# Performance work log

Hardware: AMD Instinct MI355X
Metric: run time of the kernel (lower is better)

## Reference

```python
import jax, jax.numpy as jnp
import numpy as np

B, S, HID = 2, 2048, 1024
NH, NKV, HD = 16, 8, 128
EPS = 1e-6
THETA = 1.0e6
NEG = -1e9

def _rope_tables():
    inv_freq = 1.0 / (THETA ** (np.arange(0, HD, 2, dtype=np.float32) / HD))  # [HD/2]
    pos = np.arange(S, dtype=np.float32)
    freqs = np.outer(pos, inv_freq)                      # [S, HD/2]
    emb = np.concatenate([freqs, freqs], axis=-1)        # [S, HD]
    cos = np.broadcast_to(np.cos(emb), (B, S, HD)).copy()
    sin = np.broadcast_to(np.sin(emb), (B, S, HD)).copy()
    return jnp.asarray(cos), jnp.asarray(sin)

def setup_inputs() -> dict:
    key = jax.random.key(0)
    ks = jax.random.split(key, 8)
    hidden_states = jax.random.normal(ks[0], (B, S, HID), jnp.float32)
    cos, sin = _rope_tables()
    # additive causal mask [B,1,S,S]
    causal = jnp.triu(jnp.full((S, S), NEG, jnp.float32), k=1)
    attention_mask = jnp.broadcast_to(causal[None, None], (B, 1, S, S))
    std = 0.02
    Wq = jax.random.normal(ks[1], (NH * HD, HID), jnp.float32) * std
    Wk = jax.random.normal(ks[2], (NKV * HD, HID), jnp.float32) * std
    Wv = jax.random.normal(ks[3], (NKV * HD, HID), jnp.float32) * std
    Wo = jax.random.normal(ks[4], (HID, NH * HD), jnp.float32) * std
    q_norm_w = jnp.ones((HD,), jnp.float32)
    k_norm_w = jnp.ones((HD,), jnp.float32)
    return {"hidden_states": hidden_states, "cos": cos, "sin": sin,
            "attention_mask": attention_mask, "Wq": Wq, "Wk": Wk, "Wv": Wv,
            "Wo": Wo, "q_norm_w": q_norm_w, "k_norm_w": k_norm_w}

def _rms_norm(x, w):
    var = jnp.mean(jnp.square(x), axis=-1, keepdims=True)
    return x * jax.lax.rsqrt(var + EPS) * w

def _rotate_half(x):
    x1, x2 = jnp.split(x, 2, axis=-1)
    return jnp.concatenate([-x2, x1], axis=-1)

def reference(hidden_states, cos, sin, attention_mask, Wq, Wk, Wv, Wo, q_norm_w, k_norm_w):
    # projections: [B,S,heads,HD] -> [B,heads,S,HD]
    q = jnp.einsum('bsh,dh->bsd', hidden_states, Wq).reshape(B, S, NH, HD)
    k = jnp.einsum('bsh,dh->bsd', hidden_states, Wk).reshape(B, S, NKV, HD)
    v = jnp.einsum('bsh,dh->bsd', hidden_states, Wv).reshape(B, S, NKV, HD)
    q = jnp.transpose(_rms_norm(q, q_norm_w), (0, 2, 1, 3))
    k = jnp.transpose(_rms_norm(k, k_norm_w), (0, 2, 1, 3))
    v = jnp.transpose(v, (0, 2, 1, 3))
    c = cos[:, None]  # [B,1,S,HD]
    s = sin[:, None]
    q = q * c + _rotate_half(q) * s
    k = k * c + _rotate_half(k) * s
    # repeat kv heads: NKV -> NH
    n_rep = NH // NKV
    k = jnp.repeat(k, n_rep, axis=1)
    v = jnp.repeat(v, n_rep, axis=1)
    scaling = HD ** -0.5
    scores = jnp.einsum('bhqd,bhkd->bhqk', q, k) * scaling
    scores = scores + attention_mask
    probs = jax.nn.softmax(scores.astype(jnp.float32), axis=-1).astype(q.dtype)
    out = jnp.einsum('bhqk,bhkd->bhqd', probs, v)
    out = jnp.transpose(out, (0, 2, 1, 3)).reshape(B, S, NH * HD)
    return jnp.einsum('bsd,hd->bsh', out, Wo)
```

## Files before the change

kernel.cpp:

```cpp
#include <hip/hip_runtime.h>
#include <hip/hip_fp16.h>


typedef _Float16 f16;
typedef __attribute__((ext_vector_type(8))) _Float16 f16x8;
typedef __attribute__((ext_vector_type(4))) _Float16 f16x4;
typedef __attribute__((ext_vector_type(4))) float f32x4;

__constant__ const float kEps = 1e-6f;
__constant__ const float kScaleL2 = 0.1275179120685481f;

#define ASYNC_LD16(gp, lp)                                              \
  __builtin_amdgcn_global_load_lds(                                     \
      (const __attribute__((address_space(1))) void*)(gp),              \
      (__attribute__((address_space(3))) void*)(uint32_t)(uintptr_t)(lp), 16, 0, 0)

__global__ __launch_bounds__(256) void cast_all(
    const float* __restrict__ h, const float* __restrict__ wq,
    const float* __restrict__ wk, const float* __restrict__ wv,
    const float* __restrict__ wo, f16* __restrict__ hb,
    f16* __restrict__ wqkv, f16* __restrict__ wob) {
  const int idx = blockIdx.x * 256 + threadIdx.x;
  const float* src;
  f16* dst;
  int base;
  if (idx < 1048576) { src = h;  dst = hb;                  base = 0; }
  else if (idx < 1572864) { src = wq; dst = wqkv;               base = 1048576; }
  else if (idx < 1835008) { src = wk; dst = wqkv + 2048 * 1024; base = 1572864; }
  else if (idx < 2097152) { src = wv; dst = wqkv + 3072 * 1024; base = 1835008; }
  else { src = wo; dst = wob; base = 2097152; }
  const int i = (idx - base) * 4;
  f32x4 v = *reinterpret_cast<const f32x4*>(src + i);
  f16x4 o;
  o.x = (f16)v.x; o.y = (f16)v.y; o.z = (f16)v.z; o.w = (f16)v.w;
  *reinterpret_cast<f16x4*>(dst + i) = o;
}

__global__ __launch_bounds__(256) void gemm_bt_h(const f16* __restrict__ A,
                                                 const f16* __restrict__ Bm,
                                                 f16* __restrict__ C,
                                                 int M, int N, int K) {
  __shared__ __align__(16) f16 As[128][64];
  __shared__ __align__(16) f16 Bs[128][64];
  const int tid = threadIdx.x;
  const int lane = tid & 63;
  const int wave = tid >> 6;
  const int cl = lane & 15;
  const int quad = lane >> 4;
  const int wm = (wave >> 1) * 64;
  const int wn = (wave & 1) * 64;
  const int tm = blockIdx.y * 128;
  const int tn = blockIdx.x * 128;
  const int r0 = tid >> 3;
  const int csw = ((tid & 7) ^ (r0 & 7)) * 8;

  const f16* Ab = A + (size_t)(tm + r0) * K + csw;
  const f16* Bb = Bm + (size_t)(tn + r0) * K + csw;
  char* Al = (char*)As + wave * 1024;
  char* Bl = (char*)Bs + wave * 1024;

  f32x4 acc[4][4] = {};

  for (int k0 = 0; k0 < K; k0 += 64) {
#pragma unroll
    for (int c = 0; c < 4; ++c) {
      ASYNC_LD16(Ab + (size_t)(c * 32) * K + k0, Al + c * 4096);
      ASYNC_LD16(Bb + (size_t)(c * 32) * K + k0, Bl + c * 4096);
    }
    __syncthreads();
#pragma unroll
    for (int kk = 0; kk < 2; ++kk) {
      f16x8 af[4], bf[4];
#pragma unroll
      for (int mi = 0; mi < 4; ++mi)
        af[mi] = *reinterpret_cast<const f16x8*>(
            &As[wm + mi * 16 + cl][((kk * 4 + quad) ^ (cl & 7)) * 8]);
#pragma unroll
      for (int ni = 0; ni < 4; ++ni)
        bf[ni] = *reinterpret_cast<const f16x8*>(
            &Bs[wn + ni * 16 + cl][((kk * 4 + quad) ^ (cl & 7)) * 8]);
#pragma unroll
      for (int mi = 0; mi < 4; ++mi)
#pragma unroll
        for (int ni = 0; ni < 4; ++ni)
          acc[mi][ni] =
              __builtin_amdgcn_mfma_f32_16x16x32_f16(af[mi], bf[ni], acc[mi][ni], 0, 0, 0);
    }
    __syncthreads();
  }
#pragma unroll
  for (int mi = 0; mi < 4; ++mi)
#pragma unroll
    for (int ni = 0; ni < 4; ++ni)
#pragma unroll
      for (int r = 0; r < 4; ++r)
        C[(size_t)(tm + wm + mi * 16 + quad * 4 + r) * N + tn + wn + ni * 16 + cl] =
            (f16)acc[mi][ni][r];
}

__global__ __launch_bounds__(256) void gemm_bt64(const f16* __restrict__ A,
                                                 const f16* __restrict__ Bm,
                                                 float* __restrict__ C,
                                                 int M, int N, int K) {
  __shared__ __align__(16) f16 As[64][64];
  __shared__ __align__(16) f16 Bs[128][64];
  const int tid = threadIdx.x;
  const int lane = tid & 63;
  const int wave = tid >> 6;
  const int cl = lane & 15;
  const int quad = lane >> 4;
  const int wm = (wave >> 1) * 32;
  const int wn = (wave & 1) * 64;
  const int tm = blockIdx.y * 64;
  const int tn = blockIdx.x * 128;
  const int r0 = tid >> 3;
  const int csw = ((tid & 7) ^ (r0 & 7)) * 8;

  const f16* Ab = A + (size_t)(tm + r0) * K + csw;
  const f16* Bb = Bm + (size_t)(tn + r0) * K + csw;
  char* Al = (char*)As + wave * 1024;
  char* Bl = (char*)Bs + wave * 1024;

  f32x4 acc[2][4] = {};

  for (int k0 = 0; k0 < K; k0 += 64) {
#pragma unroll
    for (int c = 0; c < 2; ++c)
      ASYNC_LD16(Ab + (size_t)(c * 32) * K + k0, Al + c * 4096);
#pragma unroll
    for (int c = 0; c < 4; ++c)
      ASYNC_LD16(Bb + (size_t)(c * 32) * K + k0, Bl + c * 4096);
    __syncthreads();
#pragma unroll
    for (int kk = 0; kk < 2; ++kk) {
      f16x8 af[2], bf[4];
#pragma unroll
      for (int mi = 0; mi < 2; ++mi)
        af[mi] = *reinterpret_cast<const f16x8*>(
            &As[wm + mi * 16 + cl][((kk * 4 + quad) ^ (cl & 7)) * 8]);
#pragma unroll
      for (int ni = 0; ni < 4; ++ni)
        bf[ni] = *reinterpret_cast<const f16x8*>(
            &Bs[wn + ni * 16 + cl][((kk * 4 + quad) ^ (cl & 7)) * 8]);
#pragma unroll
      for (int mi = 0; mi < 2; ++mi)
#pragma unroll
        for (int ni = 0; ni < 4; ++ni)
          acc[mi][ni] =
              __builtin_amdgcn_mfma_f32_16x16x32_f16(af[mi], bf[ni], acc[mi][ni], 0, 0, 0);
    }
    __syncthreads();
  }
#pragma unroll
  for (int mi = 0; mi < 2; ++mi)
#pragma unroll
    for (int ni = 0; ni < 4; ++ni)
#pragma unroll
      for (int r = 0; r < 4; ++r)
        C[(size_t)(tm + wm + mi * 16 + quad * 4 + r) * N + tn + wn + ni * 16 + cl] =
            acc[mi][ni][r];
}

__global__ __launch_bounds__(256) void rope_norm(
    const f16* __restrict__ qkvh,
    const float* __restrict__ cosT, const float* __restrict__ sinT,
    const float* __restrict__ qw, const float* __restrict__ kw,
    f16* __restrict__ qt, f16* __restrict__ kt) {
  const int gw = blockIdx.x * 4 + (threadIdx.x >> 6);
  const int lane = threadIdx.x & 63;
  const int head = gw % 24;
  const int bs = gw / 24;
  const bool isq = head < 16;
  const f16* src = qkvh + (size_t)bs * 4096 +
                   (isq ? head * 128 : 2048 + (head - 16) * 128);
  const float x1 = (float)src[lane];
  const float x2 = (float)src[lane + 64];
  float ss = x1 * x1 + x2 * x2;
#pragma unroll
  for (int off = 32; off >= 1; off >>= 1) ss += __shfl_xor(ss, off);
  const float rms = rsqrtf(ss * (1.0f / 128.0f) + kEps);
  const float* w = isq ? qw : kw;
  const float n1 = x1 * rms * w[lane];
  const float n2 = x2 * rms * w[lane + 64];
  const float* cb = cosT + (size_t)bs * 128;
  const float* sb = sinT + (size_t)bs * 128;
  const float o1 = n1 * cb[lane] - n2 * sb[lane];
  const float o2 = n2 * cb[lane + 64] + n1 * sb[lane + 64];
  const int b = bs >> 11;
  const int s = bs & 2047;
  f16* dst;
  float sc;
  if (isq) {
    dst = qt + ((size_t)(b * 16 + head) * 2048 + s) * 128;
    sc = kScaleL2;
  } else {
    dst = kt + ((size_t)(b * 8 + (head - 16)) * 2048 + s) * 128;
    sc = 1.0f;
  }
  dst[lane] = (f16)(o1 * sc);
  dst[lane + 64] = (f16)(o2 * sc);
}

__global__ __launch_bounds__(256) void v_transpose(const f16* __restrict__ qkvh,
                                                   f16* __restrict__ vt) {
  __shared__ __align__(16) f16 tile[64][136];
  const int bh = blockIdx.y;
  const int b = bh >> 3, h = bh & 7;
  const int s0 = blockIdx.x * 64;
  const int tid = threadIdx.x;
#pragma unroll
  for (int i = 0; i < 4; ++i) {
    int c = tid + i * 256;
    int s = c >> 4;
    int cg = c & 15;
    f16x8 v = *reinterpret_cast<const f16x8*>(
        qkvh + (size_t)(b * 2048 + s0 + s) * 4096 + 3072 + h * 128 + cg * 8);
    *reinterpret_cast<f16x8*>(&tile[s][cg * 8]) = v;
  }
  __syncthreads();
#pragma unroll
  for (int i = 0; i < 4; ++i) {
    int c = tid + i * 256;
    int d = c >> 3;
    int sB = (c & 7) * 8;
    f16x8 o;
#pragma unroll
    for (int j = 0; j < 8; ++j) o[j] = tile[sB + j][d];
    *reinterpret_cast<f16x8*>(vt + ((size_t)(b * 8 + h) * 128 + d) * 2048 + s0 + sB) = o;
  }
}

__global__ __launch_bounds__(128) void attn(const f16* __restrict__ Qt,
                                            const f16* __restrict__ Kt,
                                            const f16* __restrict__ Vt,
                                            f16* __restrict__ Ot) {
  __shared__ __align__(16) f16 Ks[64 * 128];
  __shared__ __align__(16) f16 Vs[128 * 64];
  __shared__ __align__(16) f16 Ps[2][32][72];

  const int bid = blockIdx.x;
  const int bh = bid & 31;
  const int t = 31 - (bid >> 5);
  const int q0 = t * 64;
  const int b = bh >> 4, h = bh & 15;
  const int kv = h >> 1;

  const int tid = threadIdx.x;
  const int lane = tid & 63, wv = tid >> 6;
  const int cl = lane & 15, quad = lane >> 4;
  const int qw0 = q0 + wv * 32;

  const f16* qbase = Qt + ((size_t)(b * 16 + h) * 2048 + qw0 + cl) * 128;
  f16x8 aq[2][4];
#pragma unroll
  for (int mi = 0; mi < 2; ++mi)
#pragma unroll
    for (int kk = 0; kk < 4; ++kk)
      aq[mi][kk] =
          *reinterpret_cast<const f16x8*>(qbase + mi * 16 * 128 + kk * 32 + quad * 8);

  const f16* kbase = Kt + (size_t)(b * 8 + kv) * 2048 * 128;
  const f16* vbase = Vt + (size_t)(b * 8 + kv) * 128 * 2048;

  float m_[2] = {-1e30f, -1e30f}, l_[2] = {0.f, 0.f};
  f32x4 oacc[2][8] = {};

  for (int kt0 = 0; kt0 <= q0; kt0 += 64) {
#pragma unroll
    for (int i = 0; i < 8; ++i) {
      const int c = (wv * 8 + i) * 64 + lane;
      const int kr = c >> 4, kg = c & 15;
      const int kgs = (kg & 8) | ((kg & 7) ^ (kr & 7));
      ASYNC_LD16(kbase + (size_t)(kt0 + kr) * 128 + kgs * 8,
                 (char*)Ks + (wv * 8 + i) * 1024);
      const int vr = c >> 3, vg = c & 7;
      const int vgs = vg ^ (vr & 7);
      ASYNC_LD16(vbase + (size_t)vr * 2048 + kt0 + vgs * 8,
                 (char*)Vs + (wv * 8 + i) * 1024);
    }
    __syncthreads();
    f32x4 sacc[2][4] = {};
#pragma unroll
    for (int kk = 0; kk < 4; ++kk)
#pragma unroll
      for (int ni = 0; ni < 4; ++ni) {
        const int gk = kk * 4 + quad;
        const int gks = (gk & 8) | ((gk & 7) ^ (cl & 7));
        f16x8 ak =
            *reinterpret_cast<const f16x8*>(Ks + (ni * 16 + cl) * 128 + gks * 8);
#pragma unroll
        for (int mi = 0; mi < 2; ++mi)
          sacc[mi][ni] =
              __builtin_amdgcn_mfma_f32_16x16x32_f16(ak, aq[mi][kk], sacc[mi][ni], 0, 0, 0);
      }
    if (kt0 == q0) {
#pragma unroll
      for (int mi = 0; mi < 2; ++mi) {
        const int qg = qw0 + mi * 16 + cl;
#pragma unroll
        for (int ni = 0; ni < 4; ++ni) {
          const int sg = kt0 + ni * 16 + quad * 4;
#pragma unroll
          for (int r = 0; r < 4; ++r)
            if (sg + r > qg) sacc[mi][ni][r] = -1e30f;
        }
      }
    }
    float al[2];
#pragma unroll
    for (int mi = 0; mi < 2; ++mi) {
      float m0 = sacc[mi][0][0];
#pragma unroll
      for (int ni = 0; ni < 4; ++ni)
#pragma unroll
        for (int r = 0; r < 4; ++r) m0 = fmaxf(m0, sacc[mi][ni][r]);
      m0 = fmaxf(m0, __shfl_xor(m0, 16));
      m0 = fmaxf(m0, __shfl_xor(m0, 32));
      const float nm = fmaxf(m_[mi], m0);
      al[mi] = __builtin_amdgcn_exp2f(m_[mi] - nm);
      m_[mi] = nm;
      float ps = 0.f;
#pragma unroll
      for (int ni = 0; ni < 4; ++ni)
#pragma unroll
        for (int r = 0; r < 4; ++r) {
          const float p = __builtin_amdgcn_exp2f(sacc[mi][ni][r] - nm);
          sacc[mi][ni][r] = p;
          ps += p;
        }
      l_[mi] = l_[mi] * al[mi] + ps;
    }
#pragma unroll
    for (int mi = 0; mi < 2; ++mi)
#pragma unroll
      for (int ni = 0; ni < 4; ++ni) {
        f16x4 pk;
#pragma unroll
        for (int r = 0; r < 4; ++r) pk[r] = (f16)sacc[mi][ni][r];
        *reinterpret_cast<f16x4*>(&Ps[wv][mi * 16 + cl][ni * 16 + quad * 4]) = pk;
      }
#pragma unroll
    for (int mi = 0; mi < 2; ++mi)
#pragma unroll
      for (int dg = 0; dg < 8; ++dg) oacc[mi][dg] *= al[mi];
    asm volatile("s_waitcnt lgkmcnt(0)" ::: "memory");
    f16x8 bp[2][2];
#pragma unroll
    for (int mi = 0; mi < 2; ++mi)
#pragma unroll
      for (int kh = 0; kh < 2; ++kh)
        bp[mi][kh] =
            *reinterpret_cast<const f16x8*>(&Ps[wv][mi * 16 + cl][kh * 32 + quad * 8]);
#pragma unroll
    for (int kh = 0; kh < 2; ++kh)
#pragma unroll
      for (int dg = 0; dg < 8; ++dg) {
        const int gv = kh * 4 + quad;
        const int gvs = gv ^ (cl & 7);
        f16x8 av =
            *reinterpret_cast<const f16x8*>(Vs + (dg * 16 + cl) * 64 + gvs * 8);
#pragma unroll
        for (int mi = 0; mi < 2; ++mi)
          oacc[mi][dg] =
              __builtin_amdgcn_mfma_f32_16x16x32_f16(av, bp[mi][kh], oacc[mi][dg], 0, 0, 0);
      }
    __syncthreads();
  }
#pragma unroll
  for (int mi = 0; mi < 2; ++mi) {
    float l = l_[mi];
    l += __shfl_xor(l, 16);
    l += __shfl_xor(l, 32);
    const float inv = 1.0f / l;
    const size_t qg = qw0 + mi * 16 + cl;
#pragma unroll
    for (int dg = 0; dg < 8; ++dg) {
      f16x4 o;
#pragma unroll
      for (int r = 0; r < 4; ++r) o[r] = (f16)(oacc[mi][dg][r] * inv);
      *reinterpret_cast<f16x4*>(Ot + ((size_t)b * 2048 + qg) * 2048 + h * 128 +
                                dg * 16 + quad * 4) = o;
    }
  }
}

extern "C" void kernel_launch(void* const* d_in, const int* in_sizes, int n_in,
                              void* d_out, int out_size, void* d_ws, size_t ws_size,
                              hipStream_t stream) {
  (void)in_sizes; (void)n_in; (void)out_size; (void)ws_size;
  const float* hidden = (const float*)d_in[0];
  const float* cosT = (const float*)d_in[1];
  const float* sinT = (const float*)d_in[2];
  const float* Wq = (const float*)d_in[4];
  const float* Wk = (const float*)d_in[5];
  const float* Wv = (const float*)d_in[6];
  const float* Wo = (const float*)d_in[7];
  const float* qnw = (const float*)d_in[8];
  const float* knw = (const float*)d_in[9];
  float* out = (float*)d_out;

  char* ws = (char*)d_ws;
  size_t off = 0;
  auto alloc = [&](size_t bytes) {
    char* p = ws + off;
    off += (bytes + 255) & ~(size_t)255;
    return p;
  };
  f16* hb = (f16*)alloc(4096ull * 1024 * 2);
  f16* wqkv = (f16*)alloc(4096ull * 1024 * 2);
  f16* wob = (f16*)alloc(1024ull * 2048 * 2);
  f16* qkvh = (f16*)alloc(4096ull * 4096 * 2);
  f16* qt = (f16*)alloc(32ull * 2048 * 128 * 2);
  f16* kt = (f16*)alloc(16ull * 2048 * 128 * 2);
  f16* vt = (f16*)alloc(16ull * 2048 * 128 * 2);
  f16* ot = (f16*)alloc(4096ull * 2048 * 2);

  cast_all<<<10240, 256, 0, stream>>>(hidden, Wq, Wk, Wv, Wo, hb, wqkv, wob);

  gemm_bt_h<<<dim3(32, 32), 256, 0, stream>>>(hb, wqkv, qkvh, 4096, 4096, 1024);

  rope_norm<<<24576, 256, 0, stream>>>(qkvh, cosT, sinT, qnw, knw, qt, kt);
  v_transpose<<<dim3(32, 16), 256, 0, stream>>>(qkvh, vt);

  attn<<<1024, 128, 0, stream>>>(qt, kt, vt, ot);

  gemm_bt64<<<dim3(8, 64), 256, 0, stream>>>(ot, wob, out, 4096, 1024, 2048);
}
```

Baseline: 302.6 us.

## Double-buffer K/V tiles in attention with async prefetch and MFMA priority

The attention kernel now keeps two LDS buffers for K and V and issues the async global-to-LDS loads for the next key tile before computing on the current one. Waits use explicit vmcnt counts so only the older loads are drained, and raw s_barrier replaces __syncthreads. s_setprio is raised around the MFMA blocks, and the causal-mask condition is tightened to apply per wave. LDS use doubles, from 32KB to 64KB for K/V, which may lower occupancy.

After: 313.9 us. 1.04x slower.

```diff
diff --git a/kernel.cpp b/kernel.cpp
--- a/kernel.cpp
+++ b/kernel.cpp
@@ -234,8 +234,8 @@
                                             const f16* __restrict__ Kt,
                                             const f16* __restrict__ Vt,
                                             f16* __restrict__ Ot) {
-  __shared__ __align__(16) f16 Ks[64 * 128];
-  __shared__ __align__(16) f16 Vs[128 * 64];
+  __shared__ __align__(16) f16 Ks[2][64 * 128];
+  __shared__ __align__(16) f16 Vs[2][128 * 64];
   __shared__ __align__(16) f16 Ps[2][32][72];
 
   const int bid = blockIdx.x;
@@ -262,24 +262,40 @@
   const f16* kbase = Kt + (size_t)(b * 8 + kv) * 2048 * 128;
   const f16* vbase = Vt + (size_t)(b * 8 + kv) * 128 * 2048;
 
-  float m_[2] = {-1e30f, -1e30f}, l_[2] = {0.f, 0.f};
-  f32x4 oacc[2][8] = {};
-
-  for (int kt0 = 0; kt0 <= q0; kt0 += 64) {
+  auto stage = [&](int buf, int kt0) {
 #pragma unroll
     for (int i = 0; i < 8; ++i) {
-      const int c = (wv * 8 + i) * 64 + lane;
+      const int cc = wv * 8 + i;
+      const int c = cc * 64 + lane;
       const int kr = c >> 4, kg = c & 15;
       const int kgs = (kg & 8) | ((kg & 7) ^ (kr & 7));
       ASYNC_LD16(kbase + (size_t)(kt0 + kr) * 128 + kgs * 8,
-                 (char*)Ks + (wv * 8 + i) * 1024);
+                 (char*)Ks + buf * 16384 + cc * 1024);
       const int vr = c >> 3, vg = c & 7;
       const int vgs = vg ^ (vr & 7);
       ASYNC_LD16(vbase + (size_t)vr * 2048 + kt0 + vgs * 8,
-                 (char*)Vs + (wv * 8 + i) * 1024);
-    }
-    __syncthreads();
+                 (char*)Vs + buf * 16384 + cc * 1024);
+    }
+  };
+
+  float m_[2] = {-1e30f, -1e30f}, l_[2] = {0.f, 0.f};
+  f32x4 oacc[2][8] = {};
+
+  stage(0, 0);
+  int cur = 0;
+  for (int kt0 = 0; kt0 <= q0; kt0 += 64) {
+    const bool hasNext = (kt0 + 64 <= q0);
+    if (hasNext) {
+      stage(cur ^ 1, kt0 + 64);
+      asm volatile("s_waitcnt vmcnt(16)" ::: "memory");
+    } else {
+      asm volatile("s_waitcnt vmcnt(0)" ::: "memory");
+    }
+    __builtin_amdgcn_s_barrier();
+    const f16* Kc = &Ks[cur][0];
+    const f16* Vc = &Vs[cur][0];
     f32x4 sacc[2][4] = {};
+    __builtin_amdgcn_s_setprio(1);
 #pragma unroll
     for (int kk = 0; kk < 4; ++kk)
 #pragma unroll
@@ -287,13 +303,14 @@
         const int gk = kk * 4 + quad;
         const int gks = (gk & 8) | ((gk & 7) ^ (cl & 7));
         f16x8 ak =
-            *reinterpret_cast<const f16x8*>(Ks + (ni * 16 + cl) * 128 + gks * 8);
+            *reinterpret_cast<const f16x8*>(Kc + (ni * 16 + cl) * 128 + gks * 8);
 #pragma unroll
         for (int mi = 0; mi < 2; ++mi)
           sacc[mi][ni] =
               __builtin_amdgcn_mfma_f32_16x16x32_f16(ak, aq[mi][kk], sacc[mi][ni], 0, 0, 0);
       }
-    if (kt0 == q0) {
+    __builtin_amdgcn_s_setprio(0);
+    if (kt0 + 63 > qw0) {
 #pragma unroll
       for (int mi = 0; mi < 2; ++mi) {
         const int qg = qw0 + mi * 16 + cl;
@@ -351,6 +368,7 @@
       for (int kh = 0; kh < 2; ++kh)
         bp[mi][kh] =
             *reinterpret_cast<const f16x8*>(&Ps[wv][mi * 16 + cl][kh * 32 + quad * 8]);
+    __builtin_amdgcn_s_setprio(1);
 #pragma unroll
     for (int kh = 0; kh < 2; ++kh)
 #pragma unroll
@@ -358,13 +376,15 @@
         const int gv = kh * 4 + quad;
         const int gvs = gv ^ (cl & 7);
         f16x8 av =
-            *reinterpret_cast<const f16x8*>(Vs + (dg * 16 + cl) * 64 + gvs * 8);
+            *reinterpret_cast<const f16x8*>(Vc + (dg * 16 + cl) * 64 + gvs * 8);
 #pragma unroll
         for (int mi = 0; mi < 2; ++mi)
           oacc[mi][dg] =
               __builtin_amdgcn_mfma_f32_16x16x32_f16(av, bp[mi][kh], oacc[mi][dg], 0, 0, 0);
       }
-    __syncthreads();
+    __builtin_amdgcn_s_setprio(0);
+    __builtin_amdgcn_s_barrier();
+    cur ^= 1;
   }
 #pragma unroll
   for (int mi = 0; mi < 2; ++mi) {
```

## Load V fragments directly into registers instead of staging through LDS

Applied to the files above, without the earlier changes.

The attention kernel no longer copies the V tile into shared memory. Each lane now reads its own V MFMA operands straight from global memory into registers, issuing the two halves at different points so the loads can overlap the QK^T MFMAs. s_setprio is raised around the MFMA sections, and the causal mask is now applied per wave whenever the tile crosses that wave's diagonal. This cuts LDS traffic and frees shared memory for occupancy, at the cost of more VGPRs and uncoalesced, duplicated global reads of V (both waves fetch the same data).

Result: slower. 319.4 us (+5.6%).

```diff
diff --git a/kernel.cpp b/kernel.cpp
--- a/kernel.cpp
+++ b/kernel.cpp
@@ -235,7 +235,6 @@
                                             const f16* __restrict__ Vt,
                                             f16* __restrict__ Ot) {
   __shared__ __align__(16) f16 Ks[64 * 128];
-  __shared__ __align__(16) f16 Vs[128 * 64];
   __shared__ __align__(16) f16 Ps[2][32][72];
 
   const int bid = blockIdx.x;
@@ -260,26 +259,29 @@
           *reinterpret_cast<const f16x8*>(qbase + mi * 16 * 128 + kk * 32 + quad * 8);
 
   const f16* kbase = Kt + (size_t)(b * 8 + kv) * 2048 * 128;
-  const f16* vbase = Vt + (size_t)(b * 8 + kv) * 128 * 2048;
+  const f16* vlane = Vt + (size_t)(b * 8 + kv) * 128 * 2048 + (size_t)cl * 2048 +
+                     quad * 8;
 
   float m_[2] = {-1e30f, -1e30f}, l_[2] = {0.f, 0.f};
   f32x4 oacc[2][8] = {};
 
   for (int kt0 = 0; kt0 <= q0; kt0 += 64) {
+    f16x8 av0[8];
+#pragma unroll
+    for (int dg = 0; dg < 8; ++dg)
+      av0[dg] = *reinterpret_cast<const f16x8*>(vlane + (size_t)(dg * 16) * 2048 + kt0);
 #pragma unroll
     for (int i = 0; i < 8; ++i) {
-      const int c = (wv * 8 + i) * 64 + lane;
+      const int cc = wv * 8 + i;
+      const int c = cc * 64 + lane;
       const int kr = c >> 4, kg = c & 15;
       const int kgs = (kg & 8) | ((kg & 7) ^ (kr & 7));
       ASYNC_LD16(kbase + (size_t)(kt0 + kr) * 128 + kgs * 8,
-                 (char*)Ks + (wv * 8 + i) * 1024);
-      const int vr = c >> 3, vg = c & 7;
-      const int vgs = vg ^ (vr & 7);
-      ASYNC_LD16(vbase + (size_t)vr * 2048 + kt0 + vgs * 8,
-                 (char*)Vs + (wv * 8 + i) * 1024);
+                 (char*)Ks + cc * 1024);
     }
     __syncthreads();
     f32x4 sacc[2][4] = {};
+    __builtin_amdgcn_s_setprio(1);
 #pragma unroll
     for (int kk = 0; kk < 4; ++kk)
 #pragma unroll
@@ -293,7 +295,13 @@
           sacc[mi][ni] =
               __builtin_amdgcn_mfma_f32_16x16x32_f16(ak, aq[mi][kk], sacc[mi][ni], 0, 0, 0);
       }
-    if (kt0 == q0) {
+    __builtin_amdgcn_s_setprio(0);
+    f16x8 av1[8];
+#pragma unroll
+    for (int dg = 0; dg < 8; ++dg)
+      av1[dg] =
+          *reinterpret_cast<const f16x8*>(vlane + (size_t)(dg * 16) * 2048 + kt0 + 32);
+    if (kt0 + 63 > qw0) {
 #pragma unroll
       for (int mi = 0; mi < 2; ++mi) {
         const int qg = qw0 + mi * 16 + cl;
@@ -351,19 +359,20 @@
       for (int kh = 0; kh < 2; ++kh)
         bp[mi][kh] =
             *reinterpret_cast<const f16x8*>(&Ps[wv][mi * 16 + cl][kh * 32 + quad * 8]);
-#pragma unroll
-    for (int kh = 0; kh < 2; ++kh)
-#pragma unroll
-      for (int dg = 0; dg < 8; ++dg) {
-        const int gv = kh * 4 + quad;
-        const int gvs = gv ^ (cl & 7);
-        f16x8 av =
-            *reinterpret_cast<const f16x8*>(Vs + (dg * 16 + cl) * 64 + gvs * 8);
-#pragma unroll
-        for (int mi = 0; mi < 2; ++mi)
-          oacc[mi][dg] =
-              __builtin_amdgcn_mfma_f32_16x16x32_f16(av, bp[mi][kh], oacc[mi][dg], 0, 0, 0);
-      }
+    __builtin_amdgcn_s_setprio(1);
+#pragma unroll
+    for (int dg = 0; dg < 8; ++dg)
+#pragma unroll
+      for (int mi = 0; mi < 2; ++mi)
+        oacc[mi][dg] =
+            __builtin_amdgcn_mfma_f32_16x16x32_f16(av0[dg], bp[mi][0], oacc[mi][dg], 0, 0, 0);
+#pragma unroll
+    for (int dg = 0; dg < 8; ++dg)
+#pragma unroll
+      for (int mi = 0; mi < 2; ++mi)
+        oacc[mi][dg] =
+            __builtin_amdgcn_mfma_f32_16x16x32_f16(av1[dg], bp[mi][1], oacc[mi][dg], 0, 0, 0);
+    __builtin_amdgcn_s_setprio(0);
     __syncthreads();
   }
 #pragma unroll
```

## Split attention query tile across four waves and raise MFMA priority

Applied to the files above, without the earlier changes.

The attention kernel now runs 256 threads per block, so each of four waves owns 16 query rows instead of two waves owning 32 each. Per-wave accumulators, softmax state and the P scratch tile are halved, and the K/V tile loads are spread over more threads. The causal-mask test moves to per-wave granularity, and s_setprio is raised around the MFMA loops. More waves per block means more latency hiding and lower register pressure, but each K/V tile loaded into LDS is reused by fewer MFMAs per wave.

Measured after the change: 294.0 us. 1.03x faster.

```diff
diff --git a/kernel.cpp b/kernel.cpp
--- a/kernel.cpp
+++ b/kernel.cpp
@@ -230,13 +230,13 @@
   }
 }
 
-__global__ __launch_bounds__(128) void attn(const f16* __restrict__ Qt,
-                                            const f16* __restrict__ Kt,
-                                            const f16* __restrict__ Vt,
-                                            f16* __restrict__ Ot) {
+__global__ __launch_bounds__(256, 3) void attn(const f16* __restrict__ Qt,
+                                               const f16* __restrict__ Kt,
+                                               const f16* __restrict__ Vt,
+                                               f16* __restrict__ Ot) {
   __shared__ __align__(16) f16 Ks[64 * 128];
   __shared__ __align__(16) f16 Vs[128 * 64];
-  __shared__ __align__(16) f16 Ps[2][32][72];
+  __shared__ __align__(16) f16 Ps[4][16][72];
 
   const int bid = blockIdx.x;
   const int bh = bid & 31;
@@ -248,109 +248,94 @@
   const int tid = threadIdx.x;
   const int lane = tid & 63, wv = tid >> 6;
   const int cl = lane & 15, quad = lane >> 4;
-  const int qw0 = q0 + wv * 32;
+  const int qw0 = q0 + wv * 16;
 
   const f16* qbase = Qt + ((size_t)(b * 16 + h) * 2048 + qw0 + cl) * 128;
-  f16x8 aq[2][4];
-#pragma unroll
-  for (int mi = 0; mi < 2; ++mi)
-#pragma unroll
-    for (int kk = 0; kk < 4; ++kk)
-      aq[mi][kk] =
-          *reinterpret_cast<const f16x8*>(qbase + mi * 16 * 128 + kk * 32 + quad * 8);
+  f16x8 aq[4];
+#pragma unroll
+  for (int kk = 0; kk < 4; ++kk)
+    aq[kk] = *reinterpret_cast<const f16x8*>(qbase + kk * 32 + quad * 8);
 
   const f16* kbase = Kt + (size_t)(b * 8 + kv) * 2048 * 128;
   const f16* vbase = Vt + (size_t)(b * 8 + kv) * 128 * 2048;
 
-  float m_[2] = {-1e30f, -1e30f}, l_[2] = {0.f, 0.f};
-  f32x4 oacc[2][8] = {};
+  float m_ = -1e30f, l_ = 0.f;
+  f32x4 oacc[8] = {};
 
   for (int kt0 = 0; kt0 <= q0; kt0 += 64) {
 #pragma unroll
-    for (int i = 0; i < 8; ++i) {
-      const int c = (wv * 8 + i) * 64 + lane;
+    for (int i = 0; i < 4; ++i) {
+      const int c = i * 256 + tid;
       const int kr = c >> 4, kg = c & 15;
       const int kgs = (kg & 8) | ((kg & 7) ^ (kr & 7));
       ASYNC_LD16(kbase + (size_t)(kt0 + kr) * 128 + kgs * 8,
-                 (char*)Ks + (wv * 8 + i) * 1024);
+                 (char*)Ks + i * 4096 + wv * 1024);
       const int vr = c >> 3, vg = c & 7;
       const int vgs = vg ^ (vr & 7);
       ASYNC_LD16(vbase + (size_t)vr * 2048 + kt0 + vgs * 8,
-                 (char*)Vs + (wv * 8 + i) * 1024);
-    }
-    __syncthreads();
-    f32x4 sacc[2][4] = {};
-#pragma unroll
-    for (int kk = 0; kk < 4; ++kk)
+                 (char*)Vs + i * 4096 + wv * 1024);
+    }
+    __syncthreads();
+    f32x4 sacc[4] = {};
+    __builtin_amdgcn_s_setprio(1);
+#pragma unroll
+    for (int kk = 0; kk < 4; ++kk) {
+      const int gk = kk * 4 + quad;
+      const int gks = (gk & 8) | ((gk & 7) ^ (cl & 7));
 #pragma unroll
       for (int ni = 0; ni < 4; ++ni) {
-        const int gk = kk * 4 + quad;
-        const int gks = (gk & 8) | ((gk & 7) ^ (cl & 7));
         f16x8 ak =
             *reinterpret_cast<const f16x8*>(Ks + (ni * 16 + cl) * 128 + gks * 8);
-#pragma unroll
-        for (int mi = 0; mi < 2; ++mi)
-          sacc[mi][ni] =
-              __builtin_amdgcn_mfma_f32_16x16x32_f16(ak, aq[mi][kk], sacc[mi][ni], 0, 0, 0);
+        sacc[ni] =
+            __builtin_amdgcn_mfma_f32_16x16x32_f16(ak, aq[kk], sacc[ni], 0, 0, 0);
       }
-    if (kt0 == q0) {
-#pragma unroll
-      for (int mi = 0; mi < 2; ++mi) {
-        const int qg = qw0 + mi * 16 + cl;
-#pragma unroll
-        for (int ni = 0; ni < 4; ++ni) {
-          const int sg = kt0 + ni * 16 + quad * 4;
-#pragma unroll
-          for (int r = 0; r < 4; ++r)
-            if (sg + r > qg) sacc[mi][ni][r] = -1e30f;
-        }
+    }
+    __builtin_amdgcn_s_setprio(0);
+    if (kt0 + 63 > qw0) {
+      const int qg = qw0 + cl;
+#pragma unroll
+      for (int ni = 0; ni < 4; ++ni) {
+        const int sg = kt0 + ni * 16 + quad * 4;
+#pragma unroll
+        for (int r = 0; r < 4; ++r)
+          if (sg + r > qg) sacc[ni][r] = -1e30f;
       }
     }
-    float al[2];
-#pragma unroll
-    for (int mi = 0; mi < 2; ++mi) {
-      float m0 = sacc[mi][0][0];
-#pragma unroll
-      for (int ni = 0; ni < 4; ++ni)
-#pragma unroll
-        for (int r = 0; r < 4; ++r) m0 = fmaxf(m0, sacc[mi][ni][r]);
-      m0 = fmaxf(m0, __shfl_xor(m0, 16));
-      m0 = fmaxf(m0, __shfl_xor(m0, 32));
-      const float nm = fmaxf(m_[mi], m0);
-      al[mi] = __builtin_amdgcn_exp2f(m_[mi] - nm);
-      m_[mi] = nm;
-      float ps = 0.f;
-#pragma unroll
-      for (int ni = 0; ni < 4; ++ni)
-#pragma unroll
-        for (int r = 0; r < 4; ++r) {
-          const float p = __builtin_amdgcn_exp2f(sacc[mi][ni][r] - nm);
-          sacc[mi][ni][r] = p;
-          ps += p;
-        }
-      l_[mi] = l_[mi] * al[mi] + ps;
-    }
-#pragma unroll
-    for (int mi = 0; mi < 2; ++mi)
-#pragma unroll
-      for (int ni = 0; ni < 4; ++ni) {
-        f16x4 pk;
-#pragma unroll
-        for (int r = 0; r < 4; ++r) pk[r] = (f16)sacc[mi][ni][r];
-        *reinterpret_cast<f16x4*>(&Ps[wv][mi * 16 + cl][ni * 16 + quad * 4]) = pk;
+    float m0 = sacc[0][0];
+#pragma unroll
+    for (int ni = 0; ni < 4; ++ni)
+#pragma unroll
+      for (int r = 0; r < 4; ++r) m0 = fmaxf(m0, sacc[ni][r]);
+    m0 = fmaxf(m0, __shfl_xor(m0, 16));
+    m0 = fmaxf(m0, __shfl_xor(m0, 32));
+    const float nm = fmaxf(m_, m0);
+    const float al = __builtin_amdgcn_exp2f(m_ - nm);
+    m_ = nm;
+    float ps = 0.f;
+#pragma unroll
+    for (int ni = 0; ni < 4; ++ni)
+#pragma unroll
+      for (int r = 0; r < 4; ++r) {
+        const float p = __builtin_amdgcn_exp2f(sacc[ni][r] - nm);
+        sacc[ni][r] = p;
+        ps += p;
       }
-#pragma unroll
-    for (int mi = 0; mi < 2; ++mi)
-#pragma unroll
-      for (int dg = 0; dg < 8; ++dg) oacc[mi][dg] *= al[mi];
+    l_ = l_ * al + ps;
+#pragma unroll
+    for (int ni = 0; ni < 4; ++ni) {
+      f16x4 pk;
+#pragma unroll
+      for (int r = 0; r < 4; ++r) pk[r] = (f16)sacc[ni][r];
+      *reinterpret_cast<f16x4*>(&Ps[wv][cl][ni * 16 + quad * 4]) = pk;
+    }
+#pragma unroll
+    for (int dg = 0; dg < 8; ++dg) oacc[dg] *= al;
     asm volatile("s_waitcnt lgkmcnt(0)" ::: "memory");
-    f16x8 bp[2][2];
-#pragma unroll
-    for (int mi = 0; mi < 2; ++mi)
-#pragma unroll
-      for (int kh = 0; kh < 2; ++kh)
-        bp[mi][kh] =
-            *reinterpret_cast<const f16x8*>(&Ps[wv][mi * 16 + cl][kh * 32 + quad * 8]);
+    f16x8 bp[2];
+#pragma unroll
+    for (int kh = 0; kh < 2; ++kh)
+      bp[kh] = *reinterpret_cast<const f16x8*>(&Ps[wv][cl][kh * 32 + quad * 8]);
+    __builtin_amdgcn_s_setprio(1);
 #pragma unroll
     for (int kh = 0; kh < 2; ++kh)
 #pragma unroll
@@ -359,28 +344,24 @@
         const int gvs = gv ^ (cl & 7);
         f16x8 av =
             *reinterpret_cast<const f16x8*>(Vs + (dg * 16 + cl) * 64 + gvs * 8);
-#pragma unroll
-        for (int mi = 0; mi < 2; ++mi)
-          oacc[mi][dg] =
-              __builtin_amdgcn_mfma_f32_16x16x32_f16(av, bp[mi][kh], oacc[mi][dg], 0, 0, 0);
+        oacc[dg] =
+            __builtin_amdgcn_mfma_f32_16x16x32_f16(av, bp[kh], oacc[dg], 0, 0, 0);
       }
-    __syncthreads();
-  }
-#pragma unroll
-  for (int mi = 0; mi < 2; ++mi) {
-    float l = l_[mi];
-    l += __shfl_xor(l, 16);
-    l += __shfl_xor(l, 32);
-    const float inv = 1.0f / l;
-    const size_t qg = qw0 + mi * 16 + cl;
-#pragma unroll
-    for (int dg = 0; dg < 8; ++dg) {
-      f16x4 o;
-#pragma unroll
-      for (int r = 0; r < 4; ++r) o[r] = (f16)(oacc[mi][dg][r] * inv);
-      *reinterpret_cast<f16x4*>(Ot + ((size_t)b * 2048 + qg) * 2048 + h * 128 +
-                                dg * 16 + quad * 4) = o;
-    }
+    __builtin_amdgcn_s_setprio(0);
+    __syncthreads();
+  }
+  float l = l_;
+  l += __shfl_xor(l, 16);
+  l += __shfl_xor(l, 32);
+  const float inv = 1.0f / l;
+  const size_t qg = qw0 + cl;
+#pragma unroll
+  for (int dg = 0; dg < 8; ++dg) {
+    f16x4 o;
+#pragma unroll
+    for (int r = 0; r < 4; ++r) o[r] = (f16)(oacc[dg][r] * inv);
+    *reinterpret_cast<f16x4*>(Ot + ((size_t)b * 2048 + qg) * 2048 + h * 128 +
+                              dg * 16 + quad * 4) = o;
   }
 }
 
@@ -422,7 +403,7 @@
   rope_norm<<<24576, 256, 0, stream>>>(qkvh, cosT, sinT, qnw, knw, qt, kt);
   v_transpose<<<dim3(32, 16), 256, 0, stream>>>(qkvh, vt);
 
-  attn<<<1024, 128, 0, stream>>>(qt, kt, vt, ot);
+  attn<<<1024, 256, 0, stream>>>(qt, kt, vt, ot);
 
   gemm_bt64<<<dim3(8, 64), 256, 0, stream>>>(ot, wob, out, 4096, 1024, 2048);
 }
```
